# Optimization experiments

Hardware: AMD Instinct MI355X
Metric: run time of the kernel (lower is better)

The kernel has to match this reference:

```python
import jax, jax.numpy as jnp
import numpy as np

B, D, C = 8192, 2048, 1000

def setup_inputs() -> dict:
    key = jax.random.key(0)
    k1, k2, k3 = jax.random.split(key, 3)
    x = jax.random.normal(k1, (B, D), dtype=jnp.float32)
    W = jax.random.normal(k2, (D, C), dtype=jnp.float32) * (1.0 / np.sqrt(D))
    b = jax.random.normal(k3, (C,), dtype=jnp.float32) * 0.01
    return {"x": x, "W": W, "b": b}

def reference(x, W, b):
    # inner classifier: logits out[b, c]
    out = jnp.dot(x, W) + b  # [B, C]
    # leave-one-out logsumexp per class, fused:
    # lse_k = logsumexp(out[:, != k]) = lse_all + log1p(-exp(out_k - lse_all))
    lse = jax.nn.logsumexp(out, axis=1, keepdims=True)  # [B, 1]
    loo = lse + jnp.log1p(-jnp.exp(out - lse))           # [B, C]
    # c_out = -loo; return c_out + out
    return out - loo
```

## Files before the change

### kernel.cpp

```cpp
#include <hip/hip_runtime.h>
#include <hip/hip_bf16.h>
#include <math.h>

#define BDIM 8192
#define DDIM 2048
#define CDIM 1000
#define NPAD 1024
#define BK   64

#define WS_BT_OFFSET  33554432ULL
#define WS_P0_OFFSET  37748736ULL
#define WS_P1_OFFSET  54132736ULL
#define WS_NEED       70516736ULL

typedef __attribute__((ext_vector_type(8))) short short8;
typedef __attribute__((ext_vector_type(4))) float floatx4;

__device__ __forceinline__ unsigned short f2bf(float f) {
    union { float f; unsigned u; } a; a.f = f;
    unsigned u = a.u;
    u = (u + 0x7fff + ((u >> 16) & 1)) >> 16;
    return (unsigned short)u;
}

__device__ __forceinline__ float bf2f(unsigned short h) {
    union { unsigned u; float f; } a; a.u = ((unsigned)h) << 16;
    return a.f;
}

__device__ __forceinline__ void async_copy16(const void* gp, void* lp) {
    __builtin_amdgcn_global_load_lds(
        (const __attribute__((address_space(1))) void*)gp,
        (__attribute__((address_space(3))) void*)lp,
        16, 0, 0);
}

__global__ __launch_bounds__(256) void cvt_kernel(
    const float* __restrict__ x, unsigned short* __restrict__ xb,
    const float* __restrict__ W, unsigned short* __restrict__ Bt)
{
    const int blk = blockIdx.x;
    const int t   = threadIdx.x;
    if (blk < 16384) {
        int i = blk * 256 + t;
        float4 v = ((const float4*)x)[i];
        ushort4 o;
        o.x = f2bf(v.x); o.y = f2bf(v.y); o.z = f2bf(v.z); o.w = f2bf(v.w);
        ((ushort4*)xb)[i] = o;
    } else {
        __shared__ float tile[32][33];
        const int b2 = blk - 16384;
        const int k0 = (b2 & 63) * 32;
        const int n0 = (b2 >> 6) * 32;
        const int tx = t & 31, ty = t >> 5;
        #pragma unroll
        for (int i = 0; i < 4; i++) {
            int k = k0 + ty + i * 8;
            int n = n0 + tx;
            tile[ty + i * 8][tx] = (n < CDIM) ? W[(size_t)k * CDIM + n] : 0.0f;
        }
        __syncthreads();
        #pragma unroll
        for (int i = 0; i < 4; i++) {
            int n = n0 + ty + i * 8;
            int k = k0 + tx;
            Bt[(size_t)n * DDIM + k] = f2bf(tile[tx][ty + i * 8]);
        }
    }
}

template <bool BF16OUT>
__device__ __forceinline__ void gemm_body(
    const unsigned short* __restrict__ A,
    const unsigned short* __restrict__ Bt,
    void* __restrict__ Cv,
    int mBase, int nBase, int kBase, int kIters,
    unsigned short* As, unsigned short* Bs)
{
    const int t    = threadIdx.x;
    const int wave = t >> 6;
    const int lane = t & 63;
    const int wm   = wave & 1;
    const int wn   = wave >> 1;
    const int quad = lane >> 4;
    const int l16  = lane & 15;

    floatx4 acc[4][4] = {};

    const int rowA = t >> 3;
    const int csw  = ((t & 7) ^ (rowA & 7)) * 16;
    const char* Ag = (const char*)A  + ((size_t)(mBase + rowA) * DDIM + kBase) * 2 + csw;
    const char* Bg = (const char*)Bt + ((size_t)(nBase + rowA) * DDIM + kBase) * 2 + csw;
    char* AsDst = (char*)As + t * 16;
    char* BsDst = (char*)Bs + t * 16;

    const int xorb0 = ((0 * 4 + quad) ^ (l16 & 7)) * 8;
    const int xorb1 = ((1 * 4 + quad) ^ (l16 & 7)) * 8;

    for (int kt = 0; kt < kIters * BK; kt += BK) {
        const char* a = Ag + kt * 2;
        const char* b = Bg + kt * 2;
        #pragma unroll
        for (int r = 0; r < 4; r++) {
            async_copy16(a + (size_t)r * 32 * DDIM * 2, AsDst + r * 4096);
            async_copy16(b + (size_t)r * 32 * DDIM * 2, BsDst + r * 4096);
        }
        __syncthreads();

        #pragma unroll
        for (int ks = 0; ks < 2; ks++) {
            const int xorb = ks ? xorb1 : xorb0;
            short8 af[4], bfr[4];
            #pragma unroll
            for (int mi = 0; mi < 4; mi++)
                af[mi] = *(const short8*)(As + (wm * 64 + mi * 16 + l16) * BK + xorb);
            #pragma unroll
            for (int ni = 0; ni < 4; ni++)
                bfr[ni] = *(const short8*)(Bs + (wn * 64 + ni * 16 + l16) * BK + xorb);
            #pragma unroll
            for (int mi = 0; mi < 4; mi++)
                #pragma unroll
                for (int ni = 0; ni < 4; ni++)
                    acc[mi][ni] = __builtin_amdgcn_mfma_f32_16x16x32_bf16(
                        af[mi], bfr[ni], acc[mi][ni], 0, 0, 0);
        }
        __syncthreads();
    }

    #pragma unroll
    for (int mi = 0; mi < 4; mi++) {
        int row0 = mBase + wm * 64 + mi * 16 + quad * 4;
        #pragma unroll
        for (int ni = 0; ni < 4; ni++) {
            int col = nBase + wn * 64 + ni * 16 + l16;
            if (col < CDIM) {
                #pragma unroll
                for (int rg = 0; rg < 4; rg++) {
                    if (BF16OUT)
                        ((unsigned short*)Cv)[(size_t)(row0 + rg) * CDIM + col] =
                            f2bf(acc[mi][ni][rg]);
                    else
                        ((float*)Cv)[(size_t)(row0 + rg) * CDIM + col] = acc[mi][ni][rg];
                }
            }
        }
    }
}

__global__ __launch_bounds__(256, 4) void gemm_splitk_kernel(
    const unsigned short* __restrict__ A,
    const unsigned short* __restrict__ Bt,
    unsigned short* __restrict__ P0, unsigned short* __restrict__ P1)
{
    __shared__ unsigned short As[128 * BK];
    __shared__ unsigned short Bs[128 * BK];

    const int L   = blockIdx.x;
    const int xcd = L & 7;
    const int s   = L >> 3;
    const int mz  = xcd * 16 + (s >> 3);
    const int n_t = s & 7;
    const int m_t = mz >> 1;
    const int z   = mz & 1;

    unsigned short* P = z ? P1 : P0;
    gemm_body<true>(A, Bt, P, m_t * 128, n_t * 128, z * (DDIM / 2), (DDIM / 2) / BK, As, Bs);
}

__global__ __launch_bounds__(256, 2) void gemm_single_kernel(
    const unsigned short* __restrict__ A,
    const unsigned short* __restrict__ Bt,
    float* __restrict__ C0)
{
    __shared__ unsigned short As[128 * BK];
    __shared__ unsigned short Bs[128 * BK];

    const int L   = blockIdx.x;
    const int xcd = L & 7;
    const int s   = L >> 3;
    const int m_t = xcd * 8 + (s >> 3);
    const int n_t = s & 7;

    gemm_body<false>(A, Bt, C0, m_t * 128, n_t * 128, 0, DDIM / BK, As, Bs);
}

__global__ __launch_bounds__(256) void lse_kernel(
    float* __restrict__ out,
    const unsigned short* P0, const unsigned short* P1,
    const float* __restrict__ bias, int split)
{
    const int row = blockIdx.x;
    const int t   = threadIdx.x;
    __shared__ float red[8];

    const bool valid = t < (CDIM / 4);
    const int c0 = t * 4;

    float4 v = make_float4(-INFINITY, -INFINITY, -INFINITY, -INFINITY);
    float4 e = make_float4(0.f, 0.f, 0.f, 0.f);
    if (valid) {
        if (split) {
            ushort4 p0 = *(const ushort4*)(P0 + (size_t)row * CDIM + c0);
            ushort4 p1 = *(const ushort4*)(P1 + (size_t)row * CDIM + c0);
            v.x = bf2f(p0.x) + bf2f(p1.x);
            v.y = bf2f(p0.y) + bf2f(p1.y);
            v.z = bf2f(p0.z) + bf2f(p1.z);
            v.w = bf2f(p0.w) + bf2f(p1.w);
        } else {
            v = *(const float4*)(out + (size_t)row * CDIM + c0);
        }
        float4 bb = *(const float4*)(bias + c0);
        v.x += bb.x; v.y += bb.y; v.z += bb.z; v.w += bb.w;
    }

    float m = fmaxf(fmaxf(v.x, v.y), fmaxf(v.z, v.w));
    #pragma unroll
    for (int off = 32; off > 0; off >>= 1)
        m = fmaxf(m, __shfl_down(m, off, 64));
    const int wave = t >> 6;
    if ((t & 63) == 0) red[wave] = m;
    __syncthreads();
    if (t == 0) red[4] = fmaxf(fmaxf(red[0], red[1]), fmaxf(red[2], red[3]));
    __syncthreads();
    const float M = red[4];

    float s = 0.f;
    if (valid) {
        e.x = expf(v.x - M); e.y = expf(v.y - M);
        e.z = expf(v.z - M); e.w = expf(v.w - M);
        s = e.x + e.y + e.z + e.w;
    }
    #pragma unroll
    for (int off = 32; off > 0; off >>= 1)
        s += __shfl_down(s, off, 64);
    if ((t & 63) == 0) red[wave] = s;
    __syncthreads();
    if (t == 0) red[4] = red[0] + red[1] + red[2] + red[3];
    __syncthreads();
    const float S    = red[4];
    const float lse  = M + logf(S);
    const float invS = 1.0f / S;

    if (valid) {
        float4 o;
        o.x = (v.x - lse) - log1pf(-e.x * invS);
        o.y = (v.y - lse) - log1pf(-e.y * invS);
        o.z = (v.z - lse) - log1pf(-e.z * invS);
        o.w = (v.w - lse) - log1pf(-e.w * invS);
        *(float4*)(out + (size_t)row * CDIM + c0) = o;
    }
}

extern "C" void kernel_launch(void* const* d_in, const int* in_sizes, int n_in,
                              void* d_out, int out_size, void* d_ws, size_t ws_size,
                              hipStream_t stream) {
    const float* x = (const float*)d_in[0];
    const float* W = (const float*)d_in[1];
    const float* b = (const float*)d_in[2];
    float* out = (float*)d_out;

    unsigned short* xb = (unsigned short*)d_ws;
    unsigned short* Bt = (unsigned short*)((char*)d_ws + WS_BT_OFFSET);
    unsigned short* P0 = (unsigned short*)((char*)d_ws + WS_P0_OFFSET);
    unsigned short* P1 = (unsigned short*)((char*)d_ws + WS_P1_OFFSET);
    const bool splitk = ws_size >= WS_NEED;

    cvt_kernel<<<18432, 256, 0, stream>>>(x, xb, W, Bt);

    if (splitk) {
        gemm_splitk_kernel<<<1024, 256, 0, stream>>>(xb, Bt, P0, P1);
        lse_kernel<<<BDIM, 256, 0, stream>>>(out, P0, P1, b, 1);
    } else {
        gemm_single_kernel<<<512, 256, 0, stream>>>(xb, Bt, out);
        lse_kernel<<<BDIM, 256, 0, stream>>>(out, nullptr, nullptr, b, 0);
    }
}
```

Baseline: 177.1 us.

## Double-buffer LDS tiles in GEMM to overlap async loads with MFMA

Converts the GEMM main loop to a two-stage LDS ping-pong. The first K tile is prefetched before the loop, and each iteration issues async copies for the next tile into the other buffer before computing on the current one. This cuts the loop to one barrier per iteration and is meant to hide global-to-LDS latency behind MFMA work. In exchange, LDS per block doubles to 64KB and the split-K kernel's launch bound drops from 4 to 2 blocks per CU, which lowers occupancy.

```diff
diff --git a/kernel.cpp b/kernel.cpp
--- a/kernel.cpp
+++ b/kernel.cpp
@@ -97,15 +97,28 @@
     const int xorb0 = ((0 * 4 + quad) ^ (l16 & 7)) * 8;
     const int xorb1 = ((1 * 4 + quad) ^ (l16 & 7)) * 8;
 
-    for (int kt = 0; kt < kIters * BK; kt += BK) {
-        const char* a = Ag + kt * 2;
-        const char* b = Bg + kt * 2;
-        #pragma unroll
-        for (int r = 0; r < 4; r++) {
-            async_copy16(a + (size_t)r * 32 * DDIM * 2, AsDst + r * 4096);
-            async_copy16(b + (size_t)r * 32 * DDIM * 2, BsDst + r * 4096);
-        }
+    #pragma unroll
+    for (int r = 0; r < 4; r++) {
+        async_copy16(Ag + (size_t)r * 32 * DDIM * 2, AsDst + r * 4096);
+        async_copy16(Bg + (size_t)r * 32 * DDIM * 2, BsDst + r * 4096);
+    }
+
+    for (int i = 0; i < kIters; i++) {
         __syncthreads();
+
+        if (i + 1 < kIters) {
+            const char* a = Ag + (size_t)(i + 1) * BK * 2;
+            const char* b = Bg + (size_t)(i + 1) * BK * 2;
+            const int bo = ((i + 1) & 1) * 16384;
+            #pragma unroll
+            for (int r = 0; r < 4; r++) {
+                async_copy16(a + (size_t)r * 32 * DDIM * 2, AsDst + bo + r * 4096);
+                async_copy16(b + (size_t)r * 32 * DDIM * 2, BsDst + bo + r * 4096);
+            }
+        }
+
+        const unsigned short* Acur = As + (i & 1) * 8192;
+        const unsigned short* Bcur = Bs + (i & 1) * 8192;
 
         #pragma unroll
         for (int ks = 0; ks < 2; ks++) {
@@ -113,10 +126,10 @@
             short8 af[4], bfr[4];
             #pragma unroll
             for (int mi = 0; mi < 4; mi++)
-                af[mi] = *(const short8*)(As + (wm * 64 + mi * 16 + l16) * BK + xorb);
+                af[mi] = *(const short8*)(Acur + (wm * 64 + mi * 16 + l16) * BK + xorb);
             #pragma unroll
             for (int ni = 0; ni < 4; ni++)
-                bfr[ni] = *(const short8*)(Bs + (wn * 64 + ni * 16 + l16) * BK + xorb);
+                bfr[ni] = *(const short8*)(Bcur + (wn * 64 + ni * 16 + l16) * BK + xorb);
             #pragma unroll
             for (int mi = 0; mi < 4; mi++)
                 #pragma unroll
@@ -124,7 +137,6 @@
                     acc[mi][ni] = __builtin_amdgcn_mfma_f32_16x16x32_bf16(
                         af[mi], bfr[ni], acc[mi][ni], 0, 0, 0);
         }
-        __syncthreads();
     }
 
     #pragma unroll
@@ -147,13 +159,13 @@
     }
 }
 
-__global__ __launch_bounds__(256, 4) void gemm_splitk_kernel(
+__global__ __launch_bounds__(256, 2) void gemm_splitk_kernel(
     const unsigned short* __restrict__ A,
     const unsigned short* __restrict__ Bt,
     unsigned short* __restrict__ P0, unsigned short* __restrict__ P1)
 {
-    __shared__ unsigned short As[128 * BK];
-    __shared__ unsigned short Bs[128 * BK];
+    __shared__ unsigned short As[2 * 128 * BK];
+    __shared__ unsigned short Bs[2 * 128 * BK];
 
     const int L   = blockIdx.x;
     const int xcd = L & 7;
@@ -172,8 +184,8 @@
     const unsigned short* __restrict__ Bt,
     float* __restrict__ C0)
 {
-    __shared__ unsigned short As[128 * BK];
-    __shared__ unsigned short Bs[128 * BK];
+    __shared__ unsigned short As[2 * 128 * BK];
+    __shared__ unsigned short Bs[2 * 128 * BK];
 
     const int L   = blockIdx.x;
     const int xcd = L & 7;
```

Result: no change. 178.8 us (+0.9%).
